# Optimization experiments

Measured on AMD Instinct MI355X. Metric: run time of the kernel, lower is better.

Reference implementation:

```python
import jax, jax.numpy as jnp
import numpy as np

N_NODES = 50000
N_EDGES = 250000
D_IN, D_HID, D_OUT = 768, 256, 2


def _sage_conv(x, src, dst, W_l, b_l, W_r, n_nodes):
    # PyG SAGEConv (aggr='mean', root_weight=True):
    #   out[i] = lin_l(mean_{j in N(i)} x[j]) + lin_r(x[i])
    msg = x[src]  # [E, d] gather of source-node features
    agg = jax.ops.segment_sum(msg, dst, num_segments=n_nodes)
    cnt = jax.ops.segment_sum(jnp.ones((src.shape[0],), x.dtype), dst,
                              num_segments=n_nodes)
    agg = agg / jnp.maximum(cnt, 1.0)[:, None]
    return agg @ W_l.T + b_l + x @ W_r.T


def setup_inputs() -> dict:
    key = jax.random.key(0)
    ks = jax.random.split(key, 7)
    x = jax.random.normal(ks[0], (N_NODES, D_IN), dtype=jnp.float32)
    edge_index = jax.random.randint(ks[1], (2, N_EDGES), 0, N_NODES,
                                    dtype=jnp.int64)
    s1 = 1.0 / np.sqrt(D_IN)
    s2 = 1.0 / np.sqrt(D_HID)
    W1_l = jax.random.uniform(ks[2], (D_HID, D_IN), jnp.float32, -s1, s1)
    W1_r = jax.random.uniform(ks[3], (D_HID, D_IN), jnp.float32, -s1, s1)
    b1 = jnp.zeros((D_HID,), jnp.float32)
    W2_l = jax.random.uniform(ks[4], (D_OUT, D_HID), jnp.float32, -s2, s2)
    W2_r = jax.random.uniform(ks[5], (D_OUT, D_HID), jnp.float32, -s2, s2)
    b2 = jnp.zeros((D_OUT,), jnp.float32)
    return {"x": x, "edge_index": edge_index,
            "W1_l": W1_l, "b1": b1, "W1_r": W1_r,
            "W2_l": W2_l, "b2": b2, "W2_r": W2_r}


def reference(x, edge_index, W1_l, b1, W1_r, W2_l, b2, W2_r):
    src, dst = edge_index[0], edge_index[1]
    n = x.shape[0]
    h = _sage_conv(x, src, dst, W1_l, b1, W1_r, n)
    h = jax.nn.relu(h)
    # dropout is identity in eval mode (deterministic reference)
    out = _sage_conv(h, src, dst, W2_l, b2, W2_r, n)
    return out
```

## Files before the change

kernel.cpp:

```cpp
#include <hip/hip_runtime.h>
#include <stdint.h>


#define D_IN  768
#define D_HID 256
#define N1    512
#define KITERS (D_IN / 32)

typedef __attribute__((ext_vector_type(8))) short short8;
typedef __attribute__((ext_vector_type(4))) float f32x4;

__device__ __forceinline__ void async_copy16(const void* g, void* l) {
  __builtin_amdgcn_global_load_lds(
      (const __attribute__((address_space(1))) unsigned int*)g,
      (__attribute__((address_space(3))) unsigned int*)l,
      16, 0, 0);
}

__device__ __forceinline__ unsigned short f2bf(float f) {
  union { float f; unsigned u; } v; v.f = f;
  unsigned r = v.u + 0x7FFFu + ((v.u >> 16) & 1u);
  return (unsigned short)(r >> 16);
}

__device__ __forceinline__ float bf2f(unsigned short b) {
  union { unsigned u; float f; } v; v.u = ((unsigned)b) << 16;
  return v.f;
}


__global__ void cvtidx_k(const void* __restrict__ eidx,
                         int* __restrict__ src32, int* __restrict__ dst32,
                         int* __restrict__ counts, int E) {
  __shared__ int flag32;
  int tid = threadIdx.x;
  int i = blockIdx.x * 256 + tid;
  unsigned v = (i < E) ? ((const unsigned int*)eidx)[2 * (size_t)i + 1] : 0u;
  unsigned long long any = __ballot(v != 0u);
  if (tid == 0) flag32 = 0;
  __syncthreads();
  if ((tid & 63) == 0 && any) flag32 = 1;
  __syncthreads();
  if (i >= E) return;
  int s, d;
  if (flag32) {
    const int* p = (const int*)eidx;
    s = p[i]; d = p[E + i];
  } else {
    const long long* p = (const long long*)eidx;
    s = (int)p[i]; d = (int)p[E + i];
  }
  src32[i] = s;
  dst32[i] = d;
  atomicAdd(&counts[d], 1);
}

__global__ void scanA_k(const int* __restrict__ counts,
                        int* __restrict__ blockSums, int M) {
  __shared__ int ts[256];
  int b = blockIdx.x, t = threadIdx.x;
  int base = b * 1024 + t * 4;
  int s = 0;
#pragma unroll
  for (int k = 0; k < 4; k++) { int i = base + k; if (i < M) s += counts[i]; }
  ts[t] = s;
  __syncthreads();
  for (int off = 128; off > 0; off >>= 1) {
    if (t < off) ts[t] += ts[t + off];
    __syncthreads();
  }
  if (t == 0) blockSums[b] = ts[0];
}

__global__ void scanC_k(const int* __restrict__ counts,
                        const int* __restrict__ bsums,
                        int* __restrict__ offs, int* __restrict__ cursor,
                        int M, int E, int nb) {
  __shared__ int ts[256];
  __shared__ int bofs;
  int b = blockIdx.x, t = threadIdx.x;
  if (t < 64) {
    int v = (t < nb) ? bsums[t] : 0;
    int orig = v;
#pragma unroll
    for (int off = 1; off < 64; off <<= 1) {
      int u = __shfl_up(v, off);
      if (t >= off) v += u;
    }
    if (t == b) bofs = v - orig;
  }
  int base = b * 1024 + t * 4;
  int v[4]; int s = 0;
#pragma unroll
  for (int k = 0; k < 4; k++) {
    int i = base + k;
    v[k] = (i < M) ? counts[i] : 0;
    s += v[k];
  }
  ts[t] = s;
  __syncthreads();
  for (int off = 1; off < 256; off <<= 1) {
    int x = (t >= off) ? ts[t - off] : 0;
    __syncthreads();
    ts[t] += x;
    __syncthreads();
  }
  int run = bofs + ts[t] - s;
#pragma unroll
  for (int k = 0; k < 4; k++) {
    int i = base + k;
    if (i < M) { offs[i] = run; cursor[i] = run; run += v[k]; }
  }
  if (b == 0 && t == 0) offs[M] = E;
}

__global__ void fill_k(const int* __restrict__ src, const int* __restrict__ dst,
                       int* __restrict__ cursor, int* __restrict__ csr, int E) {
  int i = blockIdx.x * 256 + threadIdx.x;
  if (i >= E) return;
  int pos = atomicAdd(&cursor[dst[i]], 1);
  csr[pos] = src[i];
}


__global__ void cvtw_k(const float* __restrict__ W1l, const float* __restrict__ W1r,
                       unsigned short* __restrict__ wb) {
  int idx = blockIdx.x * 256 + threadIdx.x;
  int total = N1 * (D_IN / 8);
  if (idx >= total) return;
  int row = idx / (D_IN / 8);
  int cpos = (idx % (D_IN / 8)) * 8;
  const float* p = (row < D_HID) ? (W1l + (size_t)row * D_IN + cpos)
                                 : (W1r + (size_t)(row - D_HID) * D_IN + cpos);
  float4 f0 = *(const float4*)p;
  float4 f1 = *(const float4*)(p + 4);
  short8 o;
  o[0] = (short)f2bf(f0.x); o[1] = (short)f2bf(f0.y);
  o[2] = (short)f2bf(f0.z); o[3] = (short)f2bf(f0.w);
  o[4] = (short)f2bf(f1.x); o[5] = (short)f2bf(f1.y);
  o[6] = (short)f2bf(f1.z); o[7] = (short)f2bf(f1.w);
  *(short8*)(wb + (size_t)idx * 8) = o;
}

__global__ __launch_bounds__(256) void gemm_k(
    const float* __restrict__ x,
    const unsigned short* __restrict__ wb,
    unsigned short* __restrict__ Cb, int M) {
  __shared__ unsigned short As[2][128 * 32];
  __shared__ unsigned short Bs[2][128 * 32];
  const int tid  = threadIdx.x;
  const int lane = tid & 63;
  const int wid  = tid >> 6;
  const int wr = wid >> 1, wc = wid & 1;
  const int m0 = blockIdx.y * 128;
  const int n0 = blockIdx.x * 128;
  const int l15  = lane & 15;
  const int quad = lane >> 4;

  const int arow0 = tid >> 2, akg = tid & 3;
  const int arow1 = arow0 + 64;
  const int aswz = akg | ((akg & 1) << 2);
  const float* agp0 = x + (size_t)min(m0 + arow0, M - 1) * D_IN + akg * 8;
  const float* agp1 = x + (size_t)min(m0 + arow1, M - 1) * D_IN + akg * 8;
  const int aoff0 = (arow0 >> 4) * 512 + akg * 128 + ((arow0 & 15) ^ aswz) * 8;
  const int aoff1 = (arow1 >> 4) * 512 + akg * 128 + ((arow1 & 15) ^ aswz) * 8;
  const int pquad = quad | ((quad & 1) << 2);

  const int brow = (tid >> 6) * 16 + (tid & 15);
  const int bcg  = (tid >> 4) & 3;
  const unsigned short* bgp0 = wb + (size_t)(n0 + brow) * D_IN + bcg * 8;
  const unsigned short* bgp1 = wb + (size_t)(n0 + brow + 64) * D_IN + bcg * 8;
  const int boff0 = tid * 8;
  const int boff1 = (tid + 256) * 8;

  f32x4 acc[4][4];
#pragma unroll
  for (int r = 0; r < 4; r++)
#pragma unroll
    for (int c = 0; c < 4; c++) acc[r][c] = (f32x4)0.0f;

  float4 a00 = *(const float4*)(agp0);
  float4 a01 = *(const float4*)(agp0 + 4);
  float4 a10 = *(const float4*)(agp1);
  float4 a11 = *(const float4*)(agp1 + 4);
  async_copy16(bgp0, &Bs[0][boff0]);
  async_copy16(bgp1, &Bs[0][boff1]);

  for (int it = 0; it < KITERS; ++it) {
    const int p = it & 1;
    short8 o0, o1;
    o0[0] = (short)f2bf(a00.x); o0[1] = (short)f2bf(a00.y);
    o0[2] = (short)f2bf(a00.z); o0[3] = (short)f2bf(a00.w);
    o0[4] = (short)f2bf(a01.x); o0[5] = (short)f2bf(a01.y);
    o0[6] = (short)f2bf(a01.z); o0[7] = (short)f2bf(a01.w);
    o1[0] = (short)f2bf(a10.x); o1[1] = (short)f2bf(a10.y);
    o1[2] = (short)f2bf(a10.z); o1[3] = (short)f2bf(a10.w);
    o1[4] = (short)f2bf(a11.x); o1[5] = (short)f2bf(a11.y);
    o1[6] = (short)f2bf(a11.z); o1[7] = (short)f2bf(a11.w);
    *(short8*)&As[p][aoff0] = o0;
    *(short8*)&As[p][aoff1] = o1;

    __syncthreads();

    if (it + 1 < KITERS) {
      const int k1 = (it + 1) * 32;
      a00 = *(const float4*)(agp0 + k1);
      a01 = *(const float4*)(agp0 + k1 + 4);
      a10 = *(const float4*)(agp1 + k1);
      a11 = *(const float4*)(agp1 + k1 + 4);
      async_copy16(bgp0 + k1, &Bs[p ^ 1][boff0]);
      async_copy16(bgp1 + k1, &Bs[p ^ 1][boff1]);
    }

    short8 a[4], b[4];
#pragma unroll
    for (int r = 0; r < 4; r++)
      a[r] = *(const short8*)&As[p][(wr * 4 + r) * 512 + quad * 128 + ((l15 ^ pquad)) * 8];
#pragma unroll
    for (int c = 0; c < 4; c++)
      b[c] = *(const short8*)&Bs[p][(wc * 4 + c) * 512 + quad * 128 + l15 * 8];
#pragma unroll
    for (int r = 0; r < 4; r++)
#pragma unroll
      for (int c = 0; c < 4; c++)
        acc[r][c] = __builtin_amdgcn_mfma_f32_16x16x32_bf16(a[r], b[c], acc[r][c], 0, 0, 0);
  }

  const int crow0 = m0 + wr * 64;
  const int ccol0 = n0 + wc * 64;
#pragma unroll
  for (int r = 0; r < 4; r++)
#pragma unroll
    for (int c = 0; c < 4; c++) {
      int col = ccol0 + c * 16 + l15;
#pragma unroll
      for (int reg = 0; reg < 4; reg++) {
        int row = crow0 + r * 16 + quad * 4 + reg;
        Cb[(size_t)row * N1 + col] = f2bf(acc[r][c][reg]);
      }
    }
}

__global__ void agg_l2_k(const unsigned short* __restrict__ Cb,
                         const int* __restrict__ offs, const int* __restrict__ csr,
                         const float* __restrict__ b1,
                         const float* __restrict__ W2l, const float* __restrict__ W2r,
                         float4* __restrict__ rs, int M) {
  int tid = threadIdx.x;
  int lane = tid & 63;
  int wid = tid >> 6;
  int wave = blockIdx.x * 4 + wid;
  int nw = gridDim.x * 4;
  int c = lane * 4;
  float4 bv  = *(const float4*)(b1 + c);
  float4 wl0 = *(const float4*)(W2l + c);
  float4 wl1 = *(const float4*)(W2l + D_HID + c);
  float4 wr0 = *(const float4*)(W2r + c);
  float4 wr1 = *(const float4*)(W2r + D_HID + c);
  for (int i = wave; i < M; i += nw) {
    int s = offs[i], e = offs[i + 1];
    float ax = 0.f, ay = 0.f, az = 0.f, aw = 0.f;
    for (int t = s; t < e; t++) {
      int j = csr[t];
      ushort4 v = *(const ushort4*)(Cb + (size_t)j * N1 + c);
      ax += bf2f(v.x); ay += bf2f(v.y); az += bf2f(v.z); aw += bf2f(v.w);
    }
    float inv = 1.0f / fmaxf((float)(e - s), 1.0f);
    ushort4 q = *(const ushort4*)(Cb + (size_t)i * N1 + D_HID + c);
    float h0 = fmaxf(ax * inv + bv.x + bf2f(q.x), 0.0f);
    float h1 = fmaxf(ay * inv + bv.y + bf2f(q.y), 0.0f);
    float h2 = fmaxf(az * inv + bv.z + bf2f(q.z), 0.0f);
    float h3 = fmaxf(aw * inv + bv.w + bf2f(q.w), 0.0f);
    float r0 = h0 * wl0.x + h1 * wl0.y + h2 * wl0.z + h3 * wl0.w;
    float r1 = h0 * wl1.x + h1 * wl1.y + h2 * wl1.z + h3 * wl1.w;
    float s0 = h0 * wr0.x + h1 * wr0.y + h2 * wr0.z + h3 * wr0.w;
    float s1 = h0 * wr1.x + h1 * wr1.y + h2 * wr1.z + h3 * wr1.w;
#pragma unroll
    for (int off = 32; off > 0; off >>= 1) {
      r0 += __shfl_xor(r0, off);
      r1 += __shfl_xor(r1, off);
      s0 += __shfl_xor(s0, off);
      s1 += __shfl_xor(s1, off);
    }
    if (lane == 0) rs[i] = make_float4(r0, r1, s0, s1);
  }
}

__global__ void final_k(const float4* __restrict__ rs, const int* __restrict__ offs,
                        const int* __restrict__ csr, const float* __restrict__ b2,
                        float* __restrict__ out, int M) {
  int i = blockIdx.x * 256 + threadIdx.x;
  if (i >= M) return;
  int s = offs[i], e = offs[i + 1];
  float a0 = 0.0f, a1 = 0.0f;
  for (int t = s; t < e; t++) {
    float4 v = rs[csr[t]];
    a0 += v.x; a1 += v.y;
  }
  float inv = 1.0f / fmaxf((float)(e - s), 1.0f);
  float4 me = rs[i];
  out[2 * i + 0] = a0 * inv + b2[0] + me.z;
  out[2 * i + 1] = a1 * inv + b2[1] + me.w;
}


extern "C" void kernel_launch(void* const* d_in, const int* in_sizes, int n_in,
                              void* d_out, int out_size, void* d_ws, size_t ws_size,
                              hipStream_t stream) {
  const float* x   = (const float*)d_in[0];
  const void*  eix = d_in[1];
  const float* W1l = (const float*)d_in[2];
  const float* b1  = (const float*)d_in[3];
  const float* W1r = (const float*)d_in[4];
  const float* W2l = (const float*)d_in[5];
  const float* b2  = (const float*)d_in[6];
  const float* W2r = (const float*)d_in[7];
  float* out = (float*)d_out;

  const int M  = in_sizes[0] / D_IN;
  const int E  = in_sizes[1] / 2;
  const int Mp = ((M + 127) / 128) * 128;
  const int nb = (M + 1023) / 1024;

  char* ws = (char*)d_ws;
  size_t off = 0;
  auto alloc = [&](size_t b) { size_t o = off; off += (b + 255) & ~(size_t)255; return o; };
  size_t oCounts = alloc((size_t)M * 4);
  size_t zeroBytes = (size_t)M * 4;
  size_t oOffs   = alloc((size_t)(M + 1) * 4);
  size_t oCursor = alloc((size_t)M * 4);
  size_t oCsr    = alloc((size_t)E * 4);
  size_t oSrc    = alloc((size_t)E * 4);
  size_t oDst    = alloc((size_t)E * 4);
  size_t oBSums  = alloc(64 * 4);
  size_t oWb     = alloc((size_t)N1 * D_IN * 2);
  size_t oC      = alloc((size_t)Mp * N1 * 2);
  size_t oRs     = alloc((size_t)M * 16);
  (void)ws_size; (void)n_in; (void)out_size;

  int* counts = (int*)(ws + oCounts);
  int* offs   = (int*)(ws + oOffs);
  int* cursor = (int*)(ws + oCursor);
  int* csr    = (int*)(ws + oCsr);
  int* src32  = (int*)(ws + oSrc);
  int* dst32  = (int*)(ws + oDst);
  int* bsums  = (int*)(ws + oBSums);
  unsigned short* wb = (unsigned short*)(ws + oWb);
  unsigned short* Cb = (unsigned short*)(ws + oC);
  float4* rs = (float4*)(ws + oRs);

  hipMemsetAsync(counts, 0, zeroBytes, stream);

  int gE = (E + 255) / 256;
  cvtidx_k<<<gE, 256, 0, stream>>>(eix, src32, dst32, counts, E);
  scanA_k<<<nb, 256, 0, stream>>>(counts, bsums, M);
  scanC_k<<<nb, 256, 0, stream>>>(counts, bsums, offs, cursor, M, E, nb);
  fill_k<<<gE, 256, 0, stream>>>(src32, dst32, cursor, csr, E);

  int gW = (N1 * (D_IN / 8) + 255) / 256;
  cvtw_k<<<gW, 256, 0, stream>>>(W1l, W1r, wb);

  dim3 gg(N1 / 128, Mp / 128);
  gemm_k<<<gg, 256, 0, stream>>>(x, wb, Cb, M);

  agg_l2_k<<<2048, 256, 0, stream>>>(Cb, offs, csr, b1, W2l, W2r, rs, M);
  final_k<<<(M + 255) / 256, 256, 0, stream>>>(rs, offs, csr, b2, out, M);
}
```

Before: 388.6 us.

## Load A fragments directly to registers, remap GEMM blocks per XCD, unroll gathers

The GEMM no longer stages the fp32 A tile through shared memory. Each wave loads and converts its own 32-row A fragments straight into MFMA operands and works on a 32x128 strip. Blocks are remapped so that each XCD processes a contiguous range of M-tiles across all four N-tiles, which should improve L2 reuse of x. Launch bounds now request 3 blocks per CU, and the gather loops in both aggregation kernels are unrolled by two to keep more loads in flight. The risks are uncoalesced direct global A loads, register pressure from 16 accumulators, and one-wave-per-node launches in place of a grid-stride loop.

After: 392.0 us. Within noise of the previous version (+0.9%).

```diff
diff --git a/kernel.cpp b/kernel.cpp
--- a/kernel.cpp
+++ b/kernel.cpp
@@ -142,29 +142,28 @@
   *(short8*)(wb + (size_t)idx * 8) = o;
 }
 
-__global__ __launch_bounds__(256) void gemm_k(
+__global__ __launch_bounds__(256, 3) void gemm_k(
     const float* __restrict__ x,
     const unsigned short* __restrict__ wb,
-    unsigned short* __restrict__ Cb, int M) {
-  __shared__ unsigned short As[2][128 * 32];
+    unsigned short* __restrict__ Cb, int M, int MT, int mtPerXcd) {
   __shared__ unsigned short Bs[2][128 * 32];
+
+  const int bid = blockIdx.x;
+  const int xcd = bid & 7;
+  const int j   = bid >> 3;
+  const int mt  = xcd * mtPerXcd + (j >> 2);
+  if (mt >= MT) return;
+  const int m0 = mt * 128;
+  const int n0 = (j & 3) * 128;
+
   const int tid  = threadIdx.x;
   const int lane = tid & 63;
   const int wid  = tid >> 6;
-  const int wr = wid >> 1, wc = wid & 1;
-  const int m0 = blockIdx.y * 128;
-  const int n0 = blockIdx.x * 128;
   const int l15  = lane & 15;
   const int quad = lane >> 4;
 
-  const int arow0 = tid >> 2, akg = tid & 3;
-  const int arow1 = arow0 + 64;
-  const int aswz = akg | ((akg & 1) << 2);
-  const float* agp0 = x + (size_t)min(m0 + arow0, M - 1) * D_IN + akg * 8;
-  const float* agp1 = x + (size_t)min(m0 + arow1, M - 1) * D_IN + akg * 8;
-  const int aoff0 = (arow0 >> 4) * 512 + akg * 128 + ((arow0 & 15) ^ aswz) * 8;
-  const int aoff1 = (arow1 >> 4) * 512 + akg * 128 + ((arow1 & 15) ^ aswz) * 8;
-  const int pquad = quad | ((quad & 1) << 2);
+  const float* arp0 = x + (size_t)min(m0 + wid * 32      + l15, M - 1) * D_IN + quad * 8;
+  const float* arp1 = x + (size_t)min(m0 + wid * 32 + 16 + l15, M - 1) * D_IN + quad * 8;
 
   const int brow = (tid >> 6) * 16 + (tid & 15);
   const int bcg  = (tid >> 4) & 3;
@@ -173,66 +172,61 @@
   const int boff0 = tid * 8;
   const int boff1 = (tid + 256) * 8;
 
-  f32x4 acc[4][4];
-#pragma unroll
-  for (int r = 0; r < 4; r++)
-#pragma unroll
-    for (int c = 0; c < 4; c++) acc[r][c] = (f32x4)0.0f;
-
-  float4 a00 = *(const float4*)(agp0);
-  float4 a01 = *(const float4*)(agp0 + 4);
-  float4 a10 = *(const float4*)(agp1);
-  float4 a11 = *(const float4*)(agp1 + 4);
+  f32x4 acc[2][8];
+#pragma unroll
+  for (int r = 0; r < 2; r++)
+#pragma unroll
+    for (int c = 0; c < 8; c++) acc[r][c] = (f32x4)0.0f;
+
   async_copy16(bgp0, &Bs[0][boff0]);
   async_copy16(bgp1, &Bs[0][boff1]);
+  float4 an00 = *(const float4*)(arp0);
+  float4 an01 = *(const float4*)(arp0 + 4);
+  float4 an10 = *(const float4*)(arp1);
+  float4 an11 = *(const float4*)(arp1 + 4);
 
   for (int it = 0; it < KITERS; ++it) {
     const int p = it & 1;
-    short8 o0, o1;
-    o0[0] = (short)f2bf(a00.x); o0[1] = (short)f2bf(a00.y);
-    o0[2] = (short)f2bf(a00.z); o0[3] = (short)f2bf(a00.w);
-    o0[4] = (short)f2bf(a01.x); o0[5] = (short)f2bf(a01.y);
-    o0[6] = (short)f2bf(a01.z); o0[7] = (short)f2bf(a01.w);
-    o1[0] = (short)f2bf(a10.x); o1[1] = (short)f2bf(a10.y);
-    o1[2] = (short)f2bf(a10.z); o1[3] = (short)f2bf(a10.w);
-    o1[4] = (short)f2bf(a11.x); o1[5] = (short)f2bf(a11.y);
-    o1[6] = (short)f2bf(a11.z); o1[7] = (short)f2bf(a11.w);
-    *(short8*)&As[p][aoff0] = o0;
-    *(short8*)&As[p][aoff1] = o1;
-
     __syncthreads();
-
     if (it + 1 < KITERS) {
-      const int k1 = (it + 1) * 32;
-      a00 = *(const float4*)(agp0 + k1);
-      a01 = *(const float4*)(agp0 + k1 + 4);
-      a10 = *(const float4*)(agp1 + k1);
-      a11 = *(const float4*)(agp1 + k1 + 4);
-      async_copy16(bgp0 + k1, &Bs[p ^ 1][boff0]);
-      async_copy16(bgp1 + k1, &Bs[p ^ 1][boff1]);
-    }
-
-    short8 a[4], b[4];
-#pragma unroll
-    for (int r = 0; r < 4; r++)
-      a[r] = *(const short8*)&As[p][(wr * 4 + r) * 512 + quad * 128 + ((l15 ^ pquad)) * 8];
-#pragma unroll
-    for (int c = 0; c < 4; c++)
-      b[c] = *(const short8*)&Bs[p][(wc * 4 + c) * 512 + quad * 128 + l15 * 8];
-#pragma unroll
-    for (int r = 0; r < 4; r++)
-#pragma unroll
-      for (int c = 0; c < 4; c++)
-        acc[r][c] = __builtin_amdgcn_mfma_f32_16x16x32_bf16(a[r], b[c], acc[r][c], 0, 0, 0);
-  }
-
-  const int crow0 = m0 + wr * 64;
-  const int ccol0 = n0 + wc * 64;
-#pragma unroll
-  for (int r = 0; r < 4; r++)
-#pragma unroll
-    for (int c = 0; c < 4; c++) {
-      int col = ccol0 + c * 16 + l15;
+      const int kn = (it + 1) * 32;
+      async_copy16(bgp0 + kn, &Bs[p ^ 1][boff0]);
+      async_copy16(bgp1 + kn, &Bs[p ^ 1][boff1]);
+    }
+    short8 a0, a1;
+    a0[0] = (short)f2bf(an00.x); a0[1] = (short)f2bf(an00.y);
+    a0[2] = (short)f2bf(an00.z); a0[3] = (short)f2bf(an00.w);
+    a0[4] = (short)f2bf(an01.x); a0[5] = (short)f2bf(an01.y);
+    a0[6] = (short)f2bf(an01.z); a0[7] = (short)f2bf(an01.w);
+    a1[0] = (short)f2bf(an10.x); a1[1] = (short)f2bf(an10.y);
+    a1[2] = (short)f2bf(an10.z); a1[3] = (short)f2bf(an10.w);
+    a1[4] = (short)f2bf(an11.x); a1[5] = (short)f2bf(an11.y);
+    a1[6] = (short)f2bf(an11.z); a1[7] = (short)f2bf(an11.w);
+    if (it + 1 < KITERS) {
+      const int kp = (it + 1) * 32;
+      an00 = *(const float4*)(arp0 + kp);
+      an01 = *(const float4*)(arp0 + kp + 4);
+      an10 = *(const float4*)(arp1 + kp);
+      an11 = *(const float4*)(arp1 + kp + 4);
+    }
+
+    short8 b[8];
+#pragma unroll
+    for (int c = 0; c < 8; c++)
+      b[c] = *(const short8*)&Bs[p][c * 512 + quad * 128 + l15 * 8];
+#pragma unroll
+    for (int c = 0; c < 8; c++) {
+      acc[0][c] = __builtin_amdgcn_mfma_f32_16x16x32_bf16(a0, b[c], acc[0][c], 0, 0, 0);
+      acc[1][c] = __builtin_amdgcn_mfma_f32_16x16x32_bf16(a1, b[c], acc[1][c], 0, 0, 0);
+    }
+  }
+
+  const int crow0 = m0 + wid * 32;
+#pragma unroll
+  for (int r = 0; r < 2; r++)
+#pragma unroll
+    for (int c = 0; c < 8; c++) {
+      int col = n0 + c * 16 + l15;
 #pragma unroll
       for (int reg = 0; reg < 4; reg++) {
         int row = crow0 + r * 16 + quad * 4 + reg;
@@ -249,41 +243,47 @@
   int tid = threadIdx.x;
   int lane = tid & 63;
   int wid = tid >> 6;
-  int wave = blockIdx.x * 4 + wid;
-  int nw = gridDim.x * 4;
+  int i = blockIdx.x * 4 + wid;
+  if (i >= M) return;
   int c = lane * 4;
   float4 bv  = *(const float4*)(b1 + c);
   float4 wl0 = *(const float4*)(W2l + c);
   float4 wl1 = *(const float4*)(W2l + D_HID + c);
   float4 wr0 = *(const float4*)(W2r + c);
   float4 wr1 = *(const float4*)(W2r + D_HID + c);
-  for (int i = wave; i < M; i += nw) {
-    int s = offs[i], e = offs[i + 1];
-    float ax = 0.f, ay = 0.f, az = 0.f, aw = 0.f;
-    for (int t = s; t < e; t++) {
-      int j = csr[t];
-      ushort4 v = *(const ushort4*)(Cb + (size_t)j * N1 + c);
-      ax += bf2f(v.x); ay += bf2f(v.y); az += bf2f(v.z); aw += bf2f(v.w);
-    }
-    float inv = 1.0f / fmaxf((float)(e - s), 1.0f);
-    ushort4 q = *(const ushort4*)(Cb + (size_t)i * N1 + D_HID + c);
-    float h0 = fmaxf(ax * inv + bv.x + bf2f(q.x), 0.0f);
-    float h1 = fmaxf(ay * inv + bv.y + bf2f(q.y), 0.0f);
-    float h2 = fmaxf(az * inv + bv.z + bf2f(q.z), 0.0f);
-    float h3 = fmaxf(aw * inv + bv.w + bf2f(q.w), 0.0f);
-    float r0 = h0 * wl0.x + h1 * wl0.y + h2 * wl0.z + h3 * wl0.w;
-    float r1 = h0 * wl1.x + h1 * wl1.y + h2 * wl1.z + h3 * wl1.w;
-    float s0 = h0 * wr0.x + h1 * wr0.y + h2 * wr0.z + h3 * wr0.w;
-    float s1 = h0 * wr1.x + h1 * wr1.y + h2 * wr1.z + h3 * wr1.w;
-#pragma unroll
-    for (int off = 32; off > 0; off >>= 1) {
-      r0 += __shfl_xor(r0, off);
-      r1 += __shfl_xor(r1, off);
-      s0 += __shfl_xor(s0, off);
-      s1 += __shfl_xor(s1, off);
-    }
-    if (lane == 0) rs[i] = make_float4(r0, r1, s0, s1);
-  }
+  int s = offs[i], e = offs[i + 1];
+  float ax = 0.f, ay = 0.f, az = 0.f, aw = 0.f;
+  int t = s;
+  for (; t + 2 <= e; t += 2) {
+    int j0 = csr[t], j1 = csr[t + 1];
+    ushort4 v0 = *(const ushort4*)(Cb + (size_t)j0 * N1 + c);
+    ushort4 v1 = *(const ushort4*)(Cb + (size_t)j1 * N1 + c);
+    ax += bf2f(v0.x) + bf2f(v1.x); ay += bf2f(v0.y) + bf2f(v1.y);
+    az += bf2f(v0.z) + bf2f(v1.z); aw += bf2f(v0.w) + bf2f(v1.w);
+  }
+  if (t < e) {
+    int j0 = csr[t];
+    ushort4 v0 = *(const ushort4*)(Cb + (size_t)j0 * N1 + c);
+    ax += bf2f(v0.x); ay += bf2f(v0.y); az += bf2f(v0.z); aw += bf2f(v0.w);
+  }
+  float inv = 1.0f / fmaxf((float)(e - s), 1.0f);
+  ushort4 q = *(const ushort4*)(Cb + (size_t)i * N1 + D_HID + c);
+  float h0 = fmaxf(ax * inv + bv.x + bf2f(q.x), 0.0f);
+  float h1 = fmaxf(ay * inv + bv.y + bf2f(q.y), 0.0f);
+  float h2 = fmaxf(az * inv + bv.z + bf2f(q.z), 0.0f);
+  float h3 = fmaxf(aw * inv + bv.w + bf2f(q.w), 0.0f);
+  float r0 = h0 * wl0.x + h1 * wl0.y + h2 * wl0.z + h3 * wl0.w;
+  float r1 = h0 * wl1.x + h1 * wl1.y + h2 * wl1.z + h3 * wl1.w;
+  float s0 = h0 * wr0.x + h1 * wr0.y + h2 * wr0.z + h3 * wr0.w;
+  float s1 = h0 * wr1.x + h1 * wr1.y + h2 * wr1.z + h3 * wr1.w;
+#pragma unroll
+  for (int off = 32; off > 0; off >>= 1) {
+    r0 += __shfl_xor(r0, off);
+    r1 += __shfl_xor(r1, off);
+    s0 += __shfl_xor(s0, off);
+    s1 += __shfl_xor(s1, off);
+  }
+  if (lane == 0) rs[i] = make_float4(r0, r1, s0, s1);
 }
 
 __global__ void final_k(const float4* __restrict__ rs, const int* __restrict__ offs,
@@ -293,9 +293,15 @@
   if (i >= M) return;
   int s = offs[i], e = offs[i + 1];
   float a0 = 0.0f, a1 = 0.0f;
-  for (int t = s; t < e; t++) {
-    float4 v = rs[csr[t]];
-    a0 += v.x; a1 += v.y;
+  int t = s;
+  for (; t + 2 <= e; t += 2) {
+    float4 v0 = rs[csr[t]];
+    float4 v1 = rs[csr[t + 1]];
+    a0 += v0.x + v1.x; a1 += v0.y + v1.y;
+  }
+  if (t < e) {
+    float4 v0 = rs[csr[t]];
+    a0 += v0.x; a1 += v0.y;
   }
   float inv = 1.0f / fmaxf((float)(e - s), 1.0f);
   float4 me = rs[i];
@@ -321,6 +327,9 @@
   const int E  = in_sizes[1] / 2;
   const int Mp = ((M + 127) / 128) * 128;
   const int nb = (M + 1023) / 1024;
+  const int MT = Mp / 128;
+  const int mtPerXcd = (MT + 7) / 8;
+  const int gemmBlocks = 8 * mtPerXcd * 4;
 
   char* ws = (char*)d_ws;
   size_t off = 0;
@@ -360,9 +369,8 @@
   int gW = (N1 * (D_IN / 8) + 255) / 256;
   cvtw_k<<<gW, 256, 0, stream>>>(W1l, W1r, wb);
 
-  dim3 gg(N1 / 128, Mp / 128);
-  gemm_k<<<gg, 256, 0, stream>>>(x, wb, Cb, M);
-
-  agg_l2_k<<<2048, 256, 0, stream>>>(Cb, offs, csr, b1, W2l, W2r, rs, M);
+  gemm_k<<<gemmBlocks, 256, 0, stream>>>(x, wb, Cb, M, MT, mtPerXcd);
+
+  agg_l2_k<<<(M + 3) / 4, 256, 0, stream>>>(Cb, offs, csr, b1, W2l, W2r, rs, M);
   final_k<<<(M + 255) / 256, 256, 0, stream>>>(rs, offs, csr, b2, out, M);
 }
```
